# Performance work log

Measured on AMD Instinct MI355X. Metric: run time of the kernel, lower is better.

Reference implementation:

```python
import jax, jax.numpy as jnp
import numpy as np

SEQ, BATCH, DIM = 2048, 32, 1024


def setup_inputs() -> dict:
    key = jax.random.key(0)
    k1, k2, k3, k4, k5 = jax.random.split(key, 5)
    scale = 1.0 / np.sqrt(DIM)
    return {
        "decoder_hidden": jax.random.normal(k1, (BATCH, 1, DIM), dtype=jnp.float32),
        "encoder_out": jax.random.normal(k2, (SEQ, BATCH, DIM), dtype=jnp.float32),
        "W_enc": jax.random.normal(k3, (DIM, DIM), dtype=jnp.float32) * scale,
        "W_dec": jax.random.normal(k4, (DIM, DIM), dtype=jnp.float32) * scale,
        "V_att": jax.random.normal(k5, (1, DIM), dtype=jnp.float32) * scale,
    }


def reference(decoder_hidden, encoder_out, W_enc, W_dec, V_att):
    # encoder_out: (seq, batch, dim); decoder_hidden: (batch, 1, dim)
    # torch Linear: y = x @ W.T with W of shape (out, in)
    keys = jnp.einsum('sbd,ed->bse', encoder_out, W_enc)      # (batch, seq, dim)
    query = decoder_hidden @ W_dec.T                           # (batch, 1, dim)
    scores = jnp.tanh(keys + query)                            # (batch, seq, dim)
    logits = jnp.einsum('bsd,d->bs', scores, V_att[0])         # (batch, seq)
    alpha = jax.nn.softmax(logits, axis=1)[..., None]          # (batch, seq, 1)
    # context = alpha^T @ encoder_out_permuted -> (batch, 1, dim)
    context = jnp.einsum('bs,sbd->bd', alpha[..., 0], encoder_out)[:, None, :]
    return context, jnp.transpose(alpha, (2, 0, 1))            # (1, batch, seq)
```

## Files before the change

kernel.cpp:

```cpp
#include <hip/hip_runtime.h>
#include <hip/hip_bf16.h>
#include <math.h>

#define SEQ   2048
#define BATCH 32
#define DIM   1024
#define MROWS (SEQ*BATCH)
#define NT2   4
#define NCH   16
#define NKT   16

typedef __attribute__((ext_vector_type(8))) short short8;
typedef __attribute__((ext_vector_type(8))) unsigned short u16x8;
typedef __attribute__((ext_vector_type(4))) float f32x4;

__device__ __forceinline__ unsigned short f2bf(float f) {
  unsigned u = __builtin_bit_cast(unsigned, f);
  u += 0x7FFFu + ((u >> 16) & 1u);
  return (unsigned short)(u >> 16);
}

__device__ __forceinline__ void gl16(const unsigned short* g, unsigned short* l) {
  __builtin_amdgcn_global_load_lds(
      (const __attribute__((address_space(1))) unsigned int*)g,
      (__attribute__((address_space(3))) unsigned int*)l, 16, 0, 0);
}

__global__ __launch_bounds__(256) void conv_bf16_k(const float* __restrict__ src,
                                                   unsigned short* __restrict__ dst) {
  size_t i = ((size_t)blockIdx.x * 256 + threadIdx.x) * 8;
  f32x4 a = __builtin_nontemporal_load(reinterpret_cast<const f32x4*>(src + i));
  f32x4 b = __builtin_nontemporal_load(reinterpret_cast<const f32x4*>(src + i + 4));
  u16x8 o;
  o[0] = f2bf(a[0]); o[1] = f2bf(a[1]); o[2] = f2bf(a[2]); o[3] = f2bf(a[3]);
  o[4] = f2bf(b[0]); o[5] = f2bf(b[1]); o[6] = f2bf(b[2]); o[7] = f2bf(b[3]);
  *reinterpret_cast<u16x8*>(dst + i) = o;
}

__global__ __launch_bounds__(256) void qpart_k(const float* __restrict__ dh,
                                               const float* __restrict__ Wd,
                                               float* __restrict__ qpart) {
  const int bx = blockIdx.x;
  const int eb = bx & 3;
  const int dc = bx >> 2;
  __shared__ float ldh[BATCH][128];
  const int tid = threadIdx.x;
#pragma unroll
  for (int i = 0; i < 4; ++i) {
    int idx = tid + i * 256;
    int bb = idx >> 5, d4 = idx & 31;
    float4 v = *reinterpret_cast<const float4*>(&dh[(size_t)bb * DIM + dc * 128 + d4 * 4]);
    *reinterpret_cast<float4*>(&ldh[bb][d4 * 4]) = v;
  }
  __syncthreads();
  const int e = eb * 256 + tid;
  float acc[BATCH];
#pragma unroll
  for (int b = 0; b < BATCH; ++b) acc[b] = 0.f;
  for (int d4 = 0; d4 < 32; ++d4) {
    float4 w = *reinterpret_cast<const float4*>(&Wd[(size_t)e * DIM + dc * 128 + d4 * 4]);
#pragma unroll
    for (int b = 0; b < BATCH; ++b) {
      float4 h = *reinterpret_cast<const float4*>(&ldh[b][d4 * 4]);
      acc[b] += w.x * h.x + w.y * h.y + w.z * h.z + w.w * h.w;
    }
  }
#pragma unroll
  for (int b = 0; b < BATCH; ++b)
    qpart[((size_t)dc * BATCH + b) * DIM + e] = acc[b];
}

__global__ __launch_bounds__(256) void qred_k(const float* __restrict__ qpart,
                                              float* __restrict__ q) {
  int i = blockIdx.x * 256 + threadIdx.x;
  float s = 0.f;
#pragma unroll
  for (int dc = 0; dc < 8; ++dc) s += qpart[(size_t)dc * 32768 + i];
  q[i] = s;
}

#define BARR  __builtin_amdgcn_s_barrier()
#define LGKM0 do { asm volatile("s_waitcnt lgkmcnt(0)" ::: "memory"); \
                   __builtin_amdgcn_sched_barrier(0); } while (0)
#define VMC(n) asm volatile("s_waitcnt vmcnt(" #n ")" ::: "memory")

#define STAGE_A(t, h) do {                                                        \
    const unsigned short* gb_ = Abase + (size_t)(t) * 64;                         \
    char* lb_ = arena + (((t) & 1) * 65536) + (h) * 16384;                        \
    gl16(gb_ + (size_t)(gA0 + (h) * 64) * 1024 + cSt * 8,                         \
         (unsigned short*)lb_ + w * 512);                                         \
    gl16(gb_ + (size_t)(gA0 + 128 + (h) * 64) * 1024 + cSt * 8,                   \
         (unsigned short*)(lb_ + 8192) + w * 512);                                \
  } while (0)

#define STAGE_B(t, h) do {                                                        \
    const unsigned short* gb_ = Bbase + (size_t)(t) * 64;                         \
    char* lb_ = arena + (((t) & 1) * 65536) + 32768 + (h) * 16384;                \
    gl16(gb_ + (size_t)(gB0 + (h) * 32) * 1024 + cSt * 8,                         \
         (unsigned short*)lb_ + w * 512);                                         \
    gl16(gb_ + (size_t)(gB0 + 128 + (h) * 32) * 1024 + cSt * 8,                   \
         (unsigned short*)(lb_ + 8192) + w * 512);                                \
  } while (0)

#define LOAD_A(d, MH) do {                                                        \
    const char* bA_ = arena + (d) * 65536 + (MH) * 16384;                         \
    _Pragma("unroll") for (int i_ = 0; i_ < 4; ++i_)                              \
    _Pragma("unroll") for (int ks_ = 0; ks_ < 2; ++ks_) {                         \
      int lrow_ = wr * 64 + i_ * 16 + fr;                                         \
      int lc_ = (ks_ * 4 + kq) ^ (fr & 7);                                        \
      a[i_][ks_] = *(const short8*)(bA_ + lrow_ * 128 + lc_ * 16);                \
    } } while (0)

#define LOAD_B(d, NH) do {                                                        \
    const char* bB_ = arena + (d) * 65536 + 32768 + (NH) * 16384;                 \
    _Pragma("unroll") for (int j_ = 0; j_ < 2; ++j_)                              \
    _Pragma("unroll") for (int ks_ = 0; ks_ < 2; ++ks_) {                         \
      int lrow_ = wc * 32 + j_ * 16 + fr;                                         \
      int lc_ = (ks_ * 4 + kq) ^ (fr & 7);                                        \
      b[NH][j_][ks_] = *(const short8*)(bB_ + lrow_ * 128 + lc_ * 16);            \
    } } while (0)

#define DO_QUAD(MH, NH) do {                                                      \
    __builtin_amdgcn_s_setprio(1);                                                \
    _Pragma("unroll") for (int i_ = 0; i_ < 4; ++i_)                              \
    _Pragma("unroll") for (int j_ = 0; j_ < 2; ++j_)                              \
    _Pragma("unroll") for (int ks_ = 0; ks_ < 2; ++ks_)                           \
      acc[(MH) * 4 + i_][(NH) * 2 + j_] =                                         \
          __builtin_amdgcn_mfma_f32_16x16x32_bf16(                                \
              a[i_][ks_], b[NH][j_][ks_], acc[(MH) * 4 + i_][(NH) * 2 + j_],      \
              0, 0, 0);                                                           \
    __builtin_amdgcn_s_setprio(0);                                                \
  } while (0)

__global__ __launch_bounds__(512, 2) void gemm8p(const unsigned short* __restrict__ A,
                                                 const unsigned short* __restrict__ B,
                                                 const float* __restrict__ q,
                                                 const float* __restrict__ V,
                                                 float* __restrict__ lpart) {
  __shared__ __align__(16) char arena[131072];

  const int bid = blockIdx.x;
  const int wg = (bid & 7) * 128 + (bid >> 3);
  const int mt = wg >> 2, nt = wg & 3;
  const int row0 = mt * 256, col0 = nt * 256;
  const int tid = threadIdx.x;
  const int lane = tid & 63, w = tid >> 6;
  const int wr = w >> 2, wc = w & 3;
  const int fr = lane & 15, kq = lane >> 4;

  const int lr0 = tid >> 3;
  const int cSt = (tid & 7) ^ (lr0 & 7);
  const int gA0 = lr0;
  const int gB0 = (lr0 & 31) + (lr0 >> 5) * 64;

  const unsigned short* Abase = A + (size_t)row0 * DIM;
  const unsigned short* Bbase = B + (size_t)col0 * DIM;

  f32x4 acc[8][4];
#pragma unroll
  for (int i = 0; i < 8; ++i)
#pragma unroll
    for (int j = 0; j < 4; ++j) acc[i][j] = (f32x4)(0.f);

  short8 a[4][2];
  short8 b[2][2][2];

  STAGE_A(0, 0); STAGE_B(0, 0); STAGE_A(0, 1); STAGE_B(0, 1);
  STAGE_A(1, 0); STAGE_B(1, 0);
  VMC(0);
  BARR;

#pragma unroll 1
  for (int t2 = 0; t2 < NKT; t2 += 2) {
    const bool last = (t2 == NKT - 2);
    LOAD_A(0, 0); LOAD_B(0, 0);
    STAGE_A(t2 + 1, 1);
    BARR; LGKM0; DO_QUAD(0, 0); BARR;
    LOAD_B(0, 1);
    STAGE_B(t2 + 1, 1);
    BARR; LGKM0; DO_QUAD(0, 1); BARR;
    LOAD_A(0, 1);
    if (!last) STAGE_A(t2 + 2, 0);
    BARR; LGKM0; DO_QUAD(1, 0); BARR;
    if (!last) { STAGE_B(t2 + 2, 0); VMC(4); } else { VMC(0); }
    BARR; LGKM0; DO_QUAD(1, 1); BARR;
    LOAD_A(1, 0); LOAD_B(1, 0);
    if (!last) STAGE_A(t2 + 2, 1);
    BARR; LGKM0; DO_QUAD(0, 0); BARR;
    LOAD_B(1, 1);
    if (!last) STAGE_B(t2 + 2, 1);
    BARR; LGKM0; DO_QUAD(0, 1); BARR;
    LOAD_A(1, 1);
    if (!last) STAGE_A(t2 + 3, 0);
    BARR; LGKM0; DO_QUAD(1, 0); BARR;
    if (!last) { STAGE_B(t2 + 3, 0); VMC(4); }
    BARR; LGKM0; DO_QUAD(1, 1); BARR;
  }

  __syncthreads();
  float* qld = (float*)arena;
  float* vld = (float*)(arena + 33280);
  float* red = (float*)(arena + 34304);
#pragma unroll
  for (int i = 0; i < 4; ++i) {
    int id = i * 512 + tid;
    int bb = id >> 6, e4 = id & 63;
    float4 v = *(const float4*)&q[(size_t)bb * DIM + col0 + e4 * 4];
    *(float4*)&qld[bb * 260 + e4 * 4] = v;
  }
  if (tid < 64) *(float4*)&vld[tid * 4] = *(const float4*)&V[col0 + tid * 4];
  __syncthreads();

#pragma unroll
  for (int mf = 0; mf < 8; ++mf) {
#pragma unroll
    for (int reg = 0; reg < 4; ++reg) {
      const int m_loc = wr * 128 + mf * 16 + kq * 4 + reg;
      const int bb = m_loc & 31;
      float val = 0.f;
#pragma unroll
      for (int nf = 0; nf < 4; ++nf) {
        const int el = wc * 64 + nf * 16 + fr;
        float x = acc[mf][nf][reg] + qld[bb * 260 + el];
        float g = __expf(2.f * x);
        float tnh = 1.f - 2.f * __builtin_amdgcn_rcpf(g + 1.f);
        val += tnh * vld[el];
      }
      val += __shfl_xor(val, 1); val += __shfl_xor(val, 2);
      val += __shfl_xor(val, 4); val += __shfl_xor(val, 8);
      if (fr == 0) red[wc * 256 + m_loc] = val;
    }
  }
  __syncthreads();
  if (tid < 256) {
    float s = red[tid] + red[256 + tid] + red[512 + tid] + red[768 + tid];
    lpart[(size_t)(row0 + tid) * NT2 + nt] = s;
  }
}

__global__ __launch_bounds__(256) void softmax_k(const float* __restrict__ lpart,
                                                 float* __restrict__ alpha) {
  const int b = blockIdx.x;
  __shared__ float lv[SEQ];
  __shared__ float sred[4];
  const int tid = threadIdx.x;
  float mx = -1e30f;
  for (int s = tid; s < SEQ; s += 256) {
    const float* p = &lpart[(size_t)(s * BATCH + b) * NT2];
    float v = p[0] + p[1] + p[2] + p[3];
    lv[s] = v;
    mx = fmaxf(mx, v);
  }
#pragma unroll
  for (int off = 32; off >= 1; off >>= 1) mx = fmaxf(mx, __shfl_xor(mx, off));
  if ((tid & 63) == 0) sred[tid >> 6] = mx;
  __syncthreads();
  mx = fmaxf(fmaxf(sred[0], sred[1]), fmaxf(sred[2], sred[3]));
  __syncthreads();
  float sm = 0.f;
  for (int s = tid; s < SEQ; s += 256) {
    float e = expf(lv[s] - mx);
    lv[s] = e;
    sm += e;
  }
#pragma unroll
  for (int off = 32; off >= 1; off >>= 1) sm += __shfl_xor(sm, off);
  if ((tid & 63) == 0) sred[tid >> 6] = sm;
  __syncthreads();
  const float inv = 1.f / (sred[0] + sred[1] + sred[2] + sred[3]);
  for (int s = tid; s < SEQ; s += 256)
    alpha[(size_t)b * SEQ + s] = lv[s] * inv;
}

__global__ __launch_bounds__(256) void ctx_part_k(const unsigned short* __restrict__ encbf,
                                                  const float* __restrict__ alpha,
                                                  float* __restrict__ cpart) {
  const int blk = blockIdx.x;
  const int b = blk & 31;
  const int ch = blk >> 5;
  const int tid = threadIdx.x;
  const int g = tid >> 7;
  const int d0 = (tid & 127) * 8;
  const int s0 = ch * (SEQ / NCH);
  float acc8[8];
#pragma unroll
  for (int k = 0; k < 8; ++k) acc8[k] = 0.f;
#pragma unroll 4
  for (int i = 0; i < SEQ / NCH; i += 2) {
    const int s = s0 + i + g;
    const float a = alpha[(size_t)b * SEQ + s];
    u16x8 v = *reinterpret_cast<const u16x8*>(&encbf[((size_t)s * BATCH + b) * DIM + d0]);
#pragma unroll
    for (int k = 0; k < 8; ++k) {
      float f = __builtin_bit_cast(float, (unsigned)v[k] << 16);
      acc8[k] += a * f;
    }
  }
  size_t o = ((size_t)(ch * 2 + g) * BATCH + b) * DIM + d0;
  float4 lo = {acc8[0], acc8[1], acc8[2], acc8[3]};
  float4 hi = {acc8[4], acc8[5], acc8[6], acc8[7]};
  *(float4*)&cpart[o] = lo;
  *(float4*)&cpart[o + 4] = hi;
}

__global__ __launch_bounds__(256) void ctxred_k(const float* __restrict__ cpart,
                                                float* __restrict__ out) {
  int i = blockIdx.x * 256 + threadIdx.x;
  float s = 0.f;
#pragma unroll
  for (int ch = 0; ch < 32; ++ch) s += cpart[(size_t)ch * 32768 + i];
  out[i] = s;
}

extern "C" void kernel_launch(void* const* d_in, const int* in_sizes, int n_in,
                              void* d_out, int out_size, void* d_ws, size_t ws_size,
                              hipStream_t stream) {
  const float* dh   = (const float*)d_in[0];
  const float* enc  = (const float*)d_in[1];
  const float* Wenc = (const float*)d_in[2];
  const float* Wdec = (const float*)d_in[3];
  const float* Vatt = (const float*)d_in[4];
  float* out = (float*)d_out;

  float* ws = (float*)d_ws;
  float* q      = ws;
  float* qpart  = ws + 32768;
  float* lpart  = ws + 294912;
  float* cpart  = ws + 557056;
  unsigned short* Wbf   = (unsigned short*)(ws + 1605632);
  unsigned short* encbf = (unsigned short*)(ws + 2129920);

  conv_bf16_k<<<dim3(512),   dim3(256), 0, stream>>>(Wenc, Wbf);
  qpart_k    <<<dim3(32),    dim3(256), 0, stream>>>(dh, Wdec, qpart);
  qred_k     <<<dim3(128),   dim3(256), 0, stream>>>(qpart, q);
  conv_bf16_k<<<dim3(32768), dim3(256), 0, stream>>>(enc, encbf);
  gemm8p     <<<dim3(1024),  dim3(512), 0, stream>>>(encbf, Wbf, q, Vatt, lpart);
  softmax_k  <<<dim3(BATCH),     dim3(256), 0, stream>>>(lpart, out + 32768);
  ctx_part_k <<<dim3(BATCH*NCH), dim3(256), 0, stream>>>(encbf, out + 32768, cpart);
  ctxred_k   <<<dim3(128),       dim3(256), 0, stream>>>(cpart, out);
}
```

Baseline: 274.1 us.

## Fuse encoder fp32-to-bf16 conversion into GEMM A-tile staging

```diff
diff --git a/kernel.cpp b/kernel.cpp
--- a/kernel.cpp
+++ b/kernel.cpp
@@ -29,8 +29,8 @@
 __global__ __launch_bounds__(256) void conv_bf16_k(const float* __restrict__ src,
                                                    unsigned short* __restrict__ dst) {
   size_t i = ((size_t)blockIdx.x * 256 + threadIdx.x) * 8;
-  f32x4 a = __builtin_nontemporal_load(reinterpret_cast<const f32x4*>(src + i));
-  f32x4 b = __builtin_nontemporal_load(reinterpret_cast<const f32x4*>(src + i + 4));
+  f32x4 a = *reinterpret_cast<const f32x4*>(src + i);
+  f32x4 b = *reinterpret_cast<const f32x4*>(src + i + 4);
   u16x8 o;
   o[0] = f2bf(a[0]); o[1] = f2bf(a[1]); o[2] = f2bf(a[2]); o[3] = f2bf(a[3]);
   o[4] = f2bf(b[0]); o[5] = f2bf(b[1]); o[6] = f2bf(b[2]); o[7] = f2bf(b[3]);
@@ -84,14 +84,29 @@
                    __builtin_amdgcn_sched_barrier(0); } while (0)
 #define VMC(n) asm volatile("s_waitcnt vmcnt(" #n ")" ::: "memory")
 
-#define STAGE_A(t, h) do {                                                        \
-    const unsigned short* gb_ = Abase + (size_t)(t) * 64;                         \
+#define ALOADS(P, t, h) do {                                                      \
+    const float* pa_ = Af + (size_t)(gA0 + (h) * 64) * 1024 + (t) * 64 + cSt * 8; \
+    P##0 = *(const f32x4*)pa_;                                                    \
+    P##1 = *(const f32x4*)(pa_ + 4);                                              \
+    P##2 = *(const f32x4*)(pa_ + 131072);                                         \
+    P##3 = *(const f32x4*)(pa_ + 131072 + 4);                                     \
+  } while (0)
+
+#define AWRITE_BODY(P, t, h) do {                                                 \
+    u16x8 w0_, w1_;                                                               \
+    w0_[0]=f2bf(P##0[0]); w0_[1]=f2bf(P##0[1]); w0_[2]=f2bf(P##0[2]);             \
+    w0_[3]=f2bf(P##0[3]); w0_[4]=f2bf(P##1[0]); w0_[5]=f2bf(P##1[1]);             \
+    w0_[6]=f2bf(P##1[2]); w0_[7]=f2bf(P##1[3]);                                   \
+    w1_[0]=f2bf(P##2[0]); w1_[1]=f2bf(P##2[1]); w1_[2]=f2bf(P##2[2]);             \
+    w1_[3]=f2bf(P##2[3]); w1_[4]=f2bf(P##3[0]); w1_[5]=f2bf(P##3[1]);             \
+    w1_[6]=f2bf(P##3[2]); w1_[7]=f2bf(P##3[3]);                                   \
     char* lb_ = arena + (((t) & 1) * 65536) + (h) * 16384;                        \
-    gl16(gb_ + (size_t)(gA0 + (h) * 64) * 1024 + cSt * 8,                         \
-         (unsigned short*)lb_ + w * 512);                                         \
-    gl16(gb_ + (size_t)(gA0 + 128 + (h) * 64) * 1024 + cSt * 8,                   \
-         (unsigned short*)(lb_ + 8192) + w * 512);                                \
+    *(u16x8*)(lb_ + tid * 16) = w0_;                                              \
+    *(u16x8*)(lb_ + 8192 + tid * 16) = w1_;                                       \
   } while (0)
+
+#define AWRITE(P, t, h)  do { VMC(2); AWRITE_BODY(P, t, h); } while (0)
+#define AWRITE0(P, t, h) do { VMC(0); AWRITE_BODY(P, t, h); } while (0)
 
 #define STAGE_B(t, h) do {                                                        \
     const unsigned short* gb_ = Bbase + (size_t)(t) * 64;                         \
@@ -132,7 +147,7 @@
     __builtin_amdgcn_s_setprio(0);                                                \
   } while (0)
 
-__global__ __launch_bounds__(512, 2) void gemm8p(const unsigned short* __restrict__ A,
+__global__ __launch_bounds__(512, 2) void gemm8p(const float* __restrict__ Aenc,
                                                  const unsigned short* __restrict__ B,
                                                  const float* __restrict__ q,
                                                  const float* __restrict__ V,
@@ -153,7 +168,7 @@
   const int gA0 = lr0;
   const int gB0 = (lr0 & 31) + (lr0 >> 5) * 64;
 
-  const unsigned short* Abase = A + (size_t)row0 * DIM;
+  const float* Af = Aenc + (size_t)row0 * DIM;
   const unsigned short* Bbase = B + (size_t)col0 * DIM;
 
   f32x4 acc[8][4];
@@ -164,36 +179,43 @@
 
   short8 a[4][2];
   short8 b[2][2][2];
-
-  STAGE_A(0, 0); STAGE_B(0, 0); STAGE_A(0, 1); STAGE_B(0, 1);
-  STAGE_A(1, 0); STAGE_B(1, 0);
-  VMC(0);
+  f32x4 X0, X1, X2, X3, Y0, Y1, Y2, Y3;
+
+  ALOADS(X, 0, 0); AWRITE0(X, 0, 0);
+  ALOADS(X, 0, 1); AWRITE0(X, 0, 1);
+  ALOADS(X, 1, 0); AWRITE0(X, 1, 0);
+  STAGE_B(0, 0); STAGE_B(0, 1);
+  ALOADS(X, 1, 1);
+  STAGE_B(1, 0);
+  VMC(6);
+  LGKM0;
   BARR;
 
 #pragma unroll 1
   for (int t2 = 0; t2 < NKT; t2 += 2) {
     const bool last = (t2 == NKT - 2);
     LOAD_A(0, 0); LOAD_B(0, 0);
-    STAGE_A(t2 + 1, 1);
+    AWRITE(X, t2 + 1, 1);
+    if (!last) ALOADS(Y, t2 + 2, 0);
     BARR; LGKM0; DO_QUAD(0, 0); BARR;
     LOAD_B(0, 1);
     STAGE_B(t2 + 1, 1);
     BARR; LGKM0; DO_QUAD(0, 1); BARR;
     LOAD_A(0, 1);
-    if (!last) STAGE_A(t2 + 2, 0);
+    if (!last) { AWRITE(Y, t2 + 2, 0); ALOADS(X, t2 + 2, 1); } else { VMC(0); }
     BARR; LGKM0; DO_QUAD(1, 0); BARR;
-    if (!last) { STAGE_B(t2 + 2, 0); VMC(4); } else { VMC(0); }
+    if (!last) STAGE_B(t2 + 2, 0);
     BARR; LGKM0; DO_QUAD(1, 1); BARR;
     LOAD_A(1, 0); LOAD_B(1, 0);
-    if (!last) STAGE_A(t2 + 2, 1);
+    if (!last) { AWRITE(X, t2 + 2, 1); ALOADS(Y, t2 + 3, 0); } else { VMC(0); }
     BARR; LGKM0; DO_QUAD(0, 0); BARR;
     LOAD_B(1, 1);
     if (!last) STAGE_B(t2 + 2, 1);
     BARR; LGKM0; DO_QUAD(0, 1); BARR;
     LOAD_A(1, 1);
-    if (!last) STAGE_A(t2 + 3, 0);
+    if (!last) { AWRITE(Y, t2 + 3, 0); ALOADS(X, t2 + 3, 1); } else { VMC(0); }
     BARR; LGKM0; DO_QUAD(1, 0); BARR;
-    if (!last) { STAGE_B(t2 + 3, 0); VMC(4); }
+    if (!last) STAGE_B(t2 + 3, 0);
     BARR; LGKM0; DO_QUAD(1, 1); BARR;
   }
 
@@ -272,35 +294,24 @@
     alpha[(size_t)b * SEQ + s] = lv[s] * inv;
 }
 
-__global__ __launch_bounds__(256) void ctx_part_k(const unsigned short* __restrict__ encbf,
+__global__ __launch_bounds__(256) void ctx_part_k(const float* __restrict__ enc,
                                                   const float* __restrict__ alpha,
                                                   float* __restrict__ cpart) {
   const int blk = blockIdx.x;
   const int b = blk & 31;
   const int ch = blk >> 5;
   const int tid = threadIdx.x;
-  const int g = tid >> 7;
-  const int d0 = (tid & 127) * 8;
   const int s0 = ch * (SEQ / NCH);
-  float acc8[8];
-#pragma unroll
-  for (int k = 0; k < 8; ++k) acc8[k] = 0.f;
+  float4 acc = make_float4(0.f, 0.f, 0.f, 0.f);
 #pragma unroll 4
-  for (int i = 0; i < SEQ / NCH; i += 2) {
-    const int s = s0 + i + g;
+  for (int i = 0; i < SEQ / NCH; ++i) {
+    const int s = s0 + i;
     const float a = alpha[(size_t)b * SEQ + s];
-    u16x8 v = *reinterpret_cast<const u16x8*>(&encbf[((size_t)s * BATCH + b) * DIM + d0]);
-#pragma unroll
-    for (int k = 0; k < 8; ++k) {
-      float f = __builtin_bit_cast(float, (unsigned)v[k] << 16);
-      acc8[k] += a * f;
-    }
-  }
-  size_t o = ((size_t)(ch * 2 + g) * BATCH + b) * DIM + d0;
-  float4 lo = {acc8[0], acc8[1], acc8[2], acc8[3]};
-  float4 hi = {acc8[4], acc8[5], acc8[6], acc8[7]};
-  *(float4*)&cpart[o] = lo;
-  *(float4*)&cpart[o + 4] = hi;
+    float4 v = *reinterpret_cast<const float4*>(
+        &enc[((size_t)s * BATCH + b) * DIM + tid * 4]);
+    acc.x += a * v.x; acc.y += a * v.y; acc.z += a * v.z; acc.w += a * v.w;
+  }
+  *reinterpret_cast<float4*>(&cpart[((size_t)ch * BATCH + b) * DIM + tid * 4]) = acc;
 }
 
 __global__ __launch_bounds__(256) void ctxred_k(const float* __restrict__ cpart,
@@ -308,7 +319,7 @@
   int i = blockIdx.x * 256 + threadIdx.x;
   float s = 0.f;
 #pragma unroll
-  for (int ch = 0; ch < 32; ++ch) s += cpart[(size_t)ch * 32768 + i];
+  for (int ch = 0; ch < NCH; ++ch) s += cpart[(size_t)ch * 32768 + i];
   out[i] = s;
 }
 
@@ -327,15 +338,13 @@
   float* qpart  = ws + 32768;
   float* lpart  = ws + 294912;
   float* cpart  = ws + 557056;
-  unsigned short* Wbf   = (unsigned short*)(ws + 1605632);
-  unsigned short* encbf = (unsigned short*)(ws + 2129920);
+  unsigned short* Wbf = (unsigned short*)(ws + 1081344);
 
   conv_bf16_k<<<dim3(512),   dim3(256), 0, stream>>>(Wenc, Wbf);
   qpart_k    <<<dim3(32),    dim3(256), 0, stream>>>(dh, Wdec, qpart);
   qred_k     <<<dim3(128),   dim3(256), 0, stream>>>(qpart, q);
-  conv_bf16_k<<<dim3(32768), dim3(256), 0, stream>>>(enc, encbf);
-  gemm8p     <<<dim3(1024),  dim3(512), 0, stream>>>(encbf, Wbf, q, Vatt, lpart);
+  gemm8p     <<<dim3(1024),  dim3(512), 0, stream>>>(enc, Wbf, q, Vatt, lpart);
   softmax_k  <<<dim3(BATCH),     dim3(256), 0, stream>>>(lpart, out + 32768);
-  ctx_part_k <<<dim3(BATCH*NCH), dim3(256), 0, stream>>>(encbf, out + 32768, cpart);
+  ctx_part_k <<<dim3(BATCH*NCH), dim3(256), 0, stream>>>(enc, out + 32768, cpart);
   ctxred_k   <<<dim3(128),       dim3(256), 0, stream>>>(cpart, out);
 }
```

Result: slower. 469.0 us (+71.1%).

## Double-buffer MFMA operand registers to overlap LDS reads with compute

Applied to the files above, without the earlier changes.

```diff
diff --git a/kernel.cpp b/kernel.cpp
--- a/kernel.cpp
+++ b/kernel.cpp
@@ -102,32 +102,32 @@
          (unsigned short*)(lb_ + 8192) + w * 512);                                \
   } while (0)
 
-#define LOAD_A(d, MH) do {                                                        \
+#define LOAD_A(SET, d, MH) do {                                                   \
     const char* bA_ = arena + (d) * 65536 + (MH) * 16384;                         \
     _Pragma("unroll") for (int i_ = 0; i_ < 4; ++i_)                              \
     _Pragma("unroll") for (int ks_ = 0; ks_ < 2; ++ks_) {                         \
       int lrow_ = wr * 64 + i_ * 16 + fr;                                         \
       int lc_ = (ks_ * 4 + kq) ^ (fr & 7);                                        \
-      a[i_][ks_] = *(const short8*)(bA_ + lrow_ * 128 + lc_ * 16);                \
+      SET[i_][ks_] = *(const short8*)(bA_ + lrow_ * 128 + lc_ * 16);              \
     } } while (0)
 
-#define LOAD_B(d, NH) do {                                                        \
+#define LOAD_B(SET, d, NH) do {                                                   \
     const char* bB_ = arena + (d) * 65536 + 32768 + (NH) * 16384;                 \
     _Pragma("unroll") for (int j_ = 0; j_ < 2; ++j_)                              \
     _Pragma("unroll") for (int ks_ = 0; ks_ < 2; ++ks_) {                         \
       int lrow_ = wc * 32 + j_ * 16 + fr;                                         \
       int lc_ = (ks_ * 4 + kq) ^ (fr & 7);                                        \
-      b[NH][j_][ks_] = *(const short8*)(bB_ + lrow_ * 128 + lc_ * 16);            \
+      SET[j_][ks_] = *(const short8*)(bB_ + lrow_ * 128 + lc_ * 16);              \
     } } while (0)
 
-#define DO_QUAD(MH, NH) do {                                                      \
+#define DO_QUAD(ASET, BSET, MH, NH) do {                                          \
     __builtin_amdgcn_s_setprio(1);                                                \
     _Pragma("unroll") for (int i_ = 0; i_ < 4; ++i_)                              \
     _Pragma("unroll") for (int j_ = 0; j_ < 2; ++j_)                              \
     _Pragma("unroll") for (int ks_ = 0; ks_ < 2; ++ks_)                           \
       acc[(MH) * 4 + i_][(NH) * 2 + j_] =                                         \
           __builtin_amdgcn_mfma_f32_16x16x32_bf16(                                \
-              a[i_][ks_], b[NH][j_][ks_], acc[(MH) * 4 + i_][(NH) * 2 + j_],      \
+              ASET[i_][ks_], BSET[j_][ks_], acc[(MH) * 4 + i_][(NH) * 2 + j_],    \
               0, 0, 0);                                                           \
     __builtin_amdgcn_s_setprio(0);                                                \
   } while (0)
@@ -162,39 +162,50 @@
 #pragma unroll
     for (int j = 0; j < 4; ++j) acc[i][j] = (f32x4)(0.f);
 
-  short8 a[4][2];
-  short8 b[2][2][2];
+  short8 a0[4][2], a1[4][2];
+  short8 b0[2][2], b1[2][2];
 
   STAGE_A(0, 0); STAGE_B(0, 0); STAGE_A(0, 1); STAGE_B(0, 1);
   STAGE_A(1, 0); STAGE_B(1, 0);
   VMC(0);
   BARR;
+  LOAD_B(b0, 0, 0);
 
 #pragma unroll 1
   for (int t2 = 0; t2 < NKT; t2 += 2) {
     const bool last = (t2 == NKT - 2);
-    LOAD_A(0, 0); LOAD_B(0, 0);
+    LOAD_A(a0, 0, 0);
     STAGE_A(t2 + 1, 1);
-    BARR; LGKM0; DO_QUAD(0, 0); BARR;
-    LOAD_B(0, 1);
+    BARR; LGKM0;
+    LOAD_B(b1, 0, 1);
+    DO_QUAD(a0, b0, 0, 0); BARR;
     STAGE_B(t2 + 1, 1);
-    BARR; LGKM0; DO_QUAD(0, 1); BARR;
-    LOAD_A(0, 1);
+    BARR; LGKM0;
+    LOAD_A(a1, 0, 1);
+    DO_QUAD(a0, b1, 0, 1); BARR;
     if (!last) STAGE_A(t2 + 2, 0);
-    BARR; LGKM0; DO_QUAD(1, 0); BARR;
+    BARR; LGKM0;
+    DO_QUAD(a1, b0, 1, 0); BARR;
     if (!last) { STAGE_B(t2 + 2, 0); VMC(4); } else { VMC(0); }
-    BARR; LGKM0; DO_QUAD(1, 1); BARR;
-    LOAD_A(1, 0); LOAD_B(1, 0);
+    BARR; LGKM0;
+    LOAD_B(b0, 1, 0);
+    DO_QUAD(a1, b1, 1, 1); BARR;
+    LOAD_A(a0, 1, 0);
     if (!last) STAGE_A(t2 + 2, 1);
-    BARR; LGKM0; DO_QUAD(0, 0); BARR;
-    LOAD_B(1, 1);
+    BARR; LGKM0;
+    LOAD_B(b1, 1, 1);
+    DO_QUAD(a0, b0, 0, 0); BARR;
     if (!last) STAGE_B(t2 + 2, 1);
-    BARR; LGKM0; DO_QUAD(0, 1); BARR;
-    LOAD_A(1, 1);
+    BARR; LGKM0;
+    LOAD_A(a1, 1, 1);
+    DO_QUAD(a0, b1, 0, 1); BARR;
     if (!last) STAGE_A(t2 + 3, 0);
-    BARR; LGKM0; DO_QUAD(1, 0); BARR;
+    BARR; LGKM0;
+    DO_QUAD(a1, b0, 1, 0); BARR;
     if (!last) { STAGE_B(t2 + 3, 0); VMC(4); }
-    BARR; LGKM0; DO_QUAD(1, 1); BARR;
+    BARR; LGKM0;
+    if (!last) LOAD_B(b0, 0, 0);
+    DO_QUAD(a1, b1, 1, 1); BARR;
   }
 
   __syncthreads();
```

Result: slower. 299.7 us (+9.3%).
